# Kernel optimization log

Hardware: AMD Instinct MI355X
Metric: run time of the kernel (lower is better)

The kernel has to match this reference:

```python
import jax, jax.numpy as jnp
import numpy as np


def setup_inputs() -> dict:
    key = jax.random.key(0)
    k1_key, k2_key = jax.random.split(key)
    C_OUT, C_IN, NB, K = 64, 64, 4, 15
    k1 = jax.random.normal(k1_key, (C_OUT * NB, C_IN * NB, K, K), dtype=jnp.float32)
    k2 = jax.random.normal(k2_key, (C_OUT * NB, C_IN * NB, K, K), dtype=jnp.float32)
    return {"k1": k1, "k2": k2, "n_blades": NB}


def _blade_conv(x, w):
    # x: [nb, nb, K, K] treated as NCHW batch, w: [nb, nb, K, K] treated as OIHW filter
    return jax.lax.conv(x, w, window_strides=(1, 1), padding="SAME")


def reference(k1, k2, n_blades):
    A, B, K, _ = k1.shape
    co, ci = A // n_blades, B // n_blades
    # (co*nb, ci*nb, K, K) -> (co, ci, nb, nb, K, K)
    a = k1.reshape(co, n_blades, ci, n_blades, K, K).transpose(0, 2, 1, 3, 4, 5)
    b = k2.reshape(co, n_blades, ci, n_blades, K, K).transpose(0, 2, 1, 3, 4, 5)
    # double vmap over (co, ci): each is a tiny nb x nb SAME conv
    k = jax.vmap(jax.vmap(_blade_conv))(a, b)  # (co, ci, nb, nb, K, K)
    k = k.transpose(0, 2, 1, 3, 4, 5).reshape(co * n_blades, ci * n_blades, K, K)
    return k
```

## Files before the change

### kernel.cpp

```cpp
#include <hip/hip_runtime.h>


typedef float f32x4 __attribute__((ext_vector_type(4)));
typedef __bf16 bf16x8 __attribute__((ext_vector_type(8)));

#define KS 15
#define SP 225
#define NCH 256
#define AROWS 29
#define AW 40

__device__ __forceinline__ unsigned short f2bf(float f) {
    unsigned u = __builtin_bit_cast(unsigned, f);
    u += 0x7FFFu + ((u >> 16) & 1u);
    return (unsigned short)(u >> 16);
}

__global__ __launch_bounds__(256, 4)
void blade_conv_mfma(const float* __restrict__ k1,
                     const float* __restrict__ k2,
                     float* __restrict__ out) {
    __shared__ __align__(16) unsigned char arena[16 * AROWS * AW * 2];
    unsigned short* Apad  = (unsigned short*)arena;
    float*          slabs = (float*)arena;

    const int tid  = threadIdx.x;
    const int lane = tid & 63;
    const int wid  = tid >> 6;
    const int co = blockIdx.x, ci = blockIdx.y;

    float b0[15], b1[15], b2[15], b3[15];
    {
        const size_t base = ((size_t)(co * 4) * NCH + ci * 4 + wid) * SP;
        #pragma unroll
        for (int ky = 0; ky < 15; ++ky) {
            b0[ky] = 0.f; b1[ky] = 0.f; b2[ky] = 0.f; b3[ky] = 0.f;
            if (lane < 15) {
                int p = ky * KS + lane;
                b0[ky] = k2[base + 0 * NCH * SP + p];
                b1[ky] = k2[base + 1 * NCH * SP + p];
                b2[ky] = k2[base + 2 * NCH * SP + p];
                b3[ky] = k2[base + 3 * NCH * SP + p];
            }
        }
    }

    f32x4 z = {0.f, 0.f, 0.f, 0.f};
    for (int i = tid; i < 16 * AROWS * AW / 8; i += 256) ((f32x4*)arena)[i] = z;
    __syncthreads();

    for (int idx = tid; idx < 16 * SP; idx += 256) {
        int nc = idx / SP, rem = idx % SP;
        int y = rem / KS, x = rem % KS;
        int n = nc >> 2, c = nc & 3;
        float v = k1[((size_t)((co * 4 + n) * NCH + ci * 4 + c)) * SP + rem];
        Apad[(nc * AROWS + y + 7) * AW + (x + 7)] = f2bf(v);
    }

    int srcA[15], srcB[15];
    #pragma unroll
    for (int ky = 0; ky < 15; ++ky) {
        srcA[ky] = (int)((unsigned)f2bf(b0[ky]) | ((unsigned)f2bf(b1[ky]) << 16));
        srcB[ky] = (int)((unsigned)f2bf(b2[ky]) | ((unsigned)f2bf(b3[ky]) << 16));
    }
    __syncthreads();

    f32x4 acc[4][4];
    #pragma unroll
    for (int n = 0; n < 4; ++n)
        #pragma unroll
        for (int o = 0; o < 4; ++o)
            acc[n][o] = z;

    const int yl   = lane & 15;
    const int kg   = lane >> 4;
    const int u0mx = (kg << 3) - yl;

    #pragma unroll
    for (int ky = 0; ky < 15; ++ky) {
        bf16x8 af[4];
        #pragma unroll
        for (int n = 0; n < 4; ++n) {
            const unsigned short* p =
                &Apad[((n * 4 + wid) * AROWS + yl + ky) * AW + (kg << 3)];
            af[n] = *(const bf16x8*)p;
        }
        unsigned r0[8], r1[8];
        #pragma unroll
        for (int j = 0; j < 8; ++j) {
            int a4 = (u0mx + j) << 2;
            r0[j] = (unsigned)__builtin_amdgcn_ds_bpermute(a4, srcA[ky]);
            r1[j] = (unsigned)__builtin_amdgcn_ds_bpermute(a4, srcB[ky]);
        }
        union { bf16x8 v; unsigned u[4]; } bo0, bo1, bo2, bo3;
        #pragma unroll
        for (int t = 0; t < 4; ++t) {
            bo0.u[t] = __builtin_amdgcn_perm(r0[2 * t + 1], r0[2 * t], 0x05040100u);
            bo1.u[t] = __builtin_amdgcn_perm(r0[2 * t + 1], r0[2 * t], 0x07060302u);
            bo2.u[t] = __builtin_amdgcn_perm(r1[2 * t + 1], r1[2 * t], 0x05040100u);
            bo3.u[t] = __builtin_amdgcn_perm(r1[2 * t + 1], r1[2 * t], 0x07060302u);
        }
        #pragma unroll
        for (int n = 0; n < 4; ++n) {
            acc[n][0] = __builtin_amdgcn_mfma_f32_16x16x32_bf16(af[n], bo0.v, acc[n][0], 0, 0, 0);
            acc[n][1] = __builtin_amdgcn_mfma_f32_16x16x32_bf16(af[n], bo1.v, acc[n][1], 0, 0, 0);
            acc[n][2] = __builtin_amdgcn_mfma_f32_16x16x32_bf16(af[n], bo2.v, acc[n][2], 0, 0, 0);
            acc[n][3] = __builtin_amdgcn_mfma_f32_16x16x32_bf16(af[n], bo3.v, acc[n][3], 0, 0, 0);
        }
    }

    const int xl = lane & 15;
    #pragma unroll
    for (int g = 0; g < 4; ++g) {
        __syncthreads();
        {
            float* slab = slabs + wid * 1280;
            #pragma unroll
            for (int o = 0; o < 4; ++o)
                *(f32x4*)&slab[(o * 16 + xl) * 20 + (kg << 2)] = acc[g][o];
        }
        __syncthreads();
        for (int idx = tid; idx < 4 * SP; idx += 256) {
            int o = idx / SP, rem = idx % SP;
            int yy = rem / KS, xx = rem % KS;
            int soff = (o * 16 + xx) * 20 + yy;
            float s = slabs[soff] + slabs[1280 + soff]
                    + slabs[2560 + soff] + slabs[3840 + soff];
            out[((size_t)((co * 4 + g) * NCH + ci * 4 + o)) * SP + rem] = s;
        }
    }
}

extern "C" void kernel_launch(void* const* d_in, const int* in_sizes, int n_in,
                              void* d_out, int out_size, void* d_ws, size_t ws_size,
                              hipStream_t stream) {
    (void)in_sizes; (void)n_in; (void)d_ws; (void)ws_size; (void)out_size;
    const float* k1 = (const float*)d_in[0];
    const float* k2 = (const float*)d_in[1];
    float* out = (float*)d_out;

    dim3 grid(64, 64, 1);
    dim3 block(256, 1, 1);
    hipLaunchKernelGGL(blade_conv_mfma, grid, block, 0, stream, k1, k2, out);
}
```

Baseline: 93.98 us.

## Replace bpermute weight gather with LDS lookup table and banded A layout

The per-wave ds_bpermute calls that build the B operand from register-held k2 values are replaced by a packed 64-bit bf16 table in LDS. Each lane now reads its B fragments directly with ordinary LDS loads, so k2 is loaded cooperatively across the whole block instead of by 15 lanes per wave. The padded A image is also reorganised into shared bands with a new row stride, placing two channels side by side per band to cut padding. This should reduce cross-lane permute traffic and register pressure, at the cost of more LDS capacity and possible bank conflicts on the table reads.

```diff
diff --git a/kernel.cpp b/kernel.cpp
--- a/kernel.cpp
+++ b/kernel.cpp
@@ -7,8 +7,12 @@
 #define KS 15
 #define SP 225
 #define NCH 256
-#define AROWS 29
-#define AW 40
+#define RSTRIDE 56
+#define ROWS 183
+#define APAD_SHORTS (ROWS * RSTRIDE)
+#define TBL_OFF (APAD_SHORTS * 2)
+#define TBL_UPC 496
+#define ARENA_B (TBL_OFF + 4 * TBL_UPC * 8)
 
 __device__ __forceinline__ unsigned short f2bf(float f) {
     unsigned u = __builtin_bit_cast(unsigned, f);
@@ -20,33 +24,18 @@
 void blade_conv_mfma(const float* __restrict__ k1,
                      const float* __restrict__ k2,
                      float* __restrict__ out) {
-    __shared__ __align__(16) unsigned char arena[16 * AROWS * AW * 2];
-    unsigned short* Apad  = (unsigned short*)arena;
-    float*          slabs = (float*)arena;
+    __shared__ __align__(16) unsigned char arena[ARENA_B];
+    unsigned short*     Apad  = (unsigned short*)arena;
+    unsigned long long* tbl   = (unsigned long long*)(arena + TBL_OFF);
+    float*              slabs = (float*)arena;
 
     const int tid  = threadIdx.x;
     const int lane = tid & 63;
     const int wid  = tid >> 6;
     const int co = blockIdx.x, ci = blockIdx.y;
 
-    float b0[15], b1[15], b2[15], b3[15];
-    {
-        const size_t base = ((size_t)(co * 4) * NCH + ci * 4 + wid) * SP;
-        #pragma unroll
-        for (int ky = 0; ky < 15; ++ky) {
-            b0[ky] = 0.f; b1[ky] = 0.f; b2[ky] = 0.f; b3[ky] = 0.f;
-            if (lane < 15) {
-                int p = ky * KS + lane;
-                b0[ky] = k2[base + 0 * NCH * SP + p];
-                b1[ky] = k2[base + 1 * NCH * SP + p];
-                b2[ky] = k2[base + 2 * NCH * SP + p];
-                b3[ky] = k2[base + 3 * NCH * SP + p];
-            }
-        }
-    }
-
     f32x4 z = {0.f, 0.f, 0.f, 0.f};
-    for (int i = tid; i < 16 * AROWS * AW / 8; i += 256) ((f32x4*)arena)[i] = z;
+    for (int i = tid; i < ARENA_B / 16; i += 256) ((f32x4*)arena)[i] = z;
     __syncthreads();
 
     for (int idx = tid; idx < 16 * SP; idx += 256) {
@@ -54,14 +43,22 @@
         int y = rem / KS, x = rem % KS;
         int n = nc >> 2, c = nc & 3;
         float v = k1[((size_t)((co * 4 + n) * NCH + ci * 4 + c)) * SP + rem];
-        Apad[(nc * AROWS + y + 7) * AW + (x + 7)] = f2bf(v);
+        int band = n * 2 + (c >> 1), side = c & 1;
+        Apad[(band * 22 + 7 + y) * RSTRIDE + side * 24 + 7 + x] = f2bf(v);
     }
 
-    int srcA[15], srcB[15];
-    #pragma unroll
-    for (int ky = 0; ky < 15; ++ky) {
-        srcA[ky] = (int)((unsigned)f2bf(b0[ky]) | ((unsigned)f2bf(b1[ky]) << 16));
-        srcB[ky] = (int)((unsigned)f2bf(b2[ky]) | ((unsigned)f2bf(b3[ky]) << 16));
+    for (int idx = tid; idx < 4 * SP; idx += 256) {
+        int c = idx / SP, rem = idx % SP;
+        int ky = rem / KS, kx = rem % KS;
+        size_t base = ((size_t)(co * 4) * NCH + ci * 4 + c) * SP + rem;
+        float v0 = k2[base];
+        float v1 = k2[base + (size_t)NCH * SP];
+        float v2 = k2[base + 2 * (size_t)NCH * SP];
+        float v3 = k2[base + 3 * (size_t)NCH * SP];
+        unsigned lo = (unsigned)f2bf(v0) | ((unsigned)f2bf(v1) << 16);
+        unsigned hi = (unsigned)f2bf(v2) | ((unsigned)f2bf(v3) << 16);
+        tbl[c * TBL_UPC + 32 * ky + kx + 15] =
+            (unsigned long long)lo | ((unsigned long long)hi << 32);
     }
     __syncthreads();
 
@@ -72,33 +69,34 @@
         for (int o = 0; o < 4; ++o)
             acc[n][o] = z;
 
-    const int yl   = lane & 15;
-    const int kg   = lane >> 4;
-    const int u0mx = (kg << 3) - yl;
+    const int yl    = lane & 15;
+    const int kg    = lane >> 4;
+    const int side_w = wid & 1, whalf = wid >> 1;
+    const int acol  = side_w * 24 + (kg << 3);
+    const unsigned long long* tbase =
+        &tbl[wid * TBL_UPC + (kg << 3) - yl + 15];
 
     #pragma unroll
     for (int ky = 0; ky < 15; ++ky) {
         bf16x8 af[4];
         #pragma unroll
         for (int n = 0; n < 4; ++n) {
-            const unsigned short* p =
-                &Apad[((n * 4 + wid) * AROWS + yl + ky) * AW + (kg << 3)];
-            af[n] = *(const bf16x8*)p;
+            int band = n * 2 + whalf;
+            af[n] = *(const bf16x8*)&Apad[(band * 22 + yl + ky) * RSTRIDE + acol];
         }
-        unsigned r0[8], r1[8];
+        unsigned long long q[8];
         #pragma unroll
-        for (int j = 0; j < 8; ++j) {
-            int a4 = (u0mx + j) << 2;
-            r0[j] = (unsigned)__builtin_amdgcn_ds_bpermute(a4, srcA[ky]);
-            r1[j] = (unsigned)__builtin_amdgcn_ds_bpermute(a4, srcB[ky]);
-        }
+        for (int j = 0; j < 8; ++j) q[j] = tbase[32 * ky + j];
+
         union { bf16x8 v; unsigned u[4]; } bo0, bo1, bo2, bo3;
         #pragma unroll
         for (int t = 0; t < 4; ++t) {
-            bo0.u[t] = __builtin_amdgcn_perm(r0[2 * t + 1], r0[2 * t], 0x05040100u);
-            bo1.u[t] = __builtin_amdgcn_perm(r0[2 * t + 1], r0[2 * t], 0x07060302u);
-            bo2.u[t] = __builtin_amdgcn_perm(r1[2 * t + 1], r1[2 * t], 0x05040100u);
-            bo3.u[t] = __builtin_amdgcn_perm(r1[2 * t + 1], r1[2 * t], 0x07060302u);
+            unsigned a0 = (unsigned)q[2 * t],         a1 = (unsigned)q[2 * t + 1];
+            unsigned b0 = (unsigned)(q[2 * t] >> 32), b1 = (unsigned)(q[2 * t + 1] >> 32);
+            bo0.u[t] = __builtin_amdgcn_perm(a1, a0, 0x05040100u);
+            bo1.u[t] = __builtin_amdgcn_perm(a1, a0, 0x07060302u);
+            bo2.u[t] = __builtin_amdgcn_perm(b1, b0, 0x05040100u);
+            bo3.u[t] = __builtin_amdgcn_perm(b1, b0, 0x07060302u);
         }
         #pragma unroll
         for (int n = 0; n < 4; ++n) {
```

New measurement: 77.52 us. 17.5% less time.
